# Performance work log

Hardware: AMD Instinct MI355X
Metric: run time of the kernel (lower is better)

The kernel has to match this reference:

```python
import jax, jax.numpy as jnp
import numpy as np

GENOMES, BATCH, SEQ, EMBED = 8, 2, 2048, 1024
HEADS, KV_HEADS = 16, 4
HEAD_DIM = EMBED // HEADS  # 64
RATIO = HEADS // KV_HEADS  # 4
CONSTANT = 10000.0


def _rope_tables(seq_len, head_dim, constant):
    theta = constant ** (-2.0 * jnp.arange(0, head_dim, 2, dtype=jnp.float32) / head_dim)
    angles = jnp.arange(seq_len, dtype=jnp.float32)[:, None] * theta[None, :]  # [S, hd/2]
    return jnp.cos(angles), jnp.sin(angles)


def _apply_rope(x, cos, sin):
    # x: [g,b,s,h,hd]; treat last dim as hd/2 complex pairs, rotate by angle per (s, pair)
    g, b, s, h, hd = x.shape
    xr = x.reshape(g, b, s, h, hd // 2, 2)
    x0, x1 = xr[..., 0], xr[..., 1]
    c = cos[None, None, :, None, :]
    sn = sin[None, None, :, None, :]
    o0 = x0 * c - x1 * sn
    o1 = x0 * sn + x1 * c
    return jnp.stack([o0, o1], axis=-1).reshape(g, b, s, h, hd)


def setup_inputs() -> dict:
    key = jax.random.key(0)
    ks = jax.random.split(key, 5)
    scale = 0.02
    return {
        "tensor": jax.random.normal(ks[0], (GENOMES, BATCH, SEQ, EMBED), dtype=jnp.float32),
        "Wq": jax.random.normal(ks[1], (GENOMES, EMBED, HEADS * HEAD_DIM), dtype=jnp.float32) * scale,
        "Wk": jax.random.normal(ks[2], (GENOMES, EMBED, KV_HEADS * HEAD_DIM), dtype=jnp.float32) * scale,
        "Wv": jax.random.normal(ks[3], (GENOMES, EMBED, KV_HEADS * HEAD_DIM), dtype=jnp.float32) * scale,
        "Wo": jax.random.normal(ks[4], (GENOMES, EMBED, EMBED), dtype=jnp.float32) * scale,
    }


def reference(tensor, Wq, Wk, Wv, Wo):
    g, b, s, _ = tensor.shape
    cos, sin = _rope_tables(SEQ, HEAD_DIM, CONSTANT)
    # per-genome linear projections
    q = jnp.einsum('gbsi,gio->gbso', tensor, Wq).reshape(g, b, s, HEADS, HEAD_DIM)
    k = jnp.einsum('gbsi,gio->gbso', tensor, Wk).reshape(g, b, s, KV_HEADS, HEAD_DIM)
    v = jnp.einsum('gbsi,gio->gbso', tensor, Wv).reshape(g, b, s, KV_HEADS, HEAD_DIM)
    q = _apply_rope(q, cos, sin)
    k = _apply_rope(k, cos, sin)
    # repeat_kv: [g,b,s,kvh,hd] -> [g,b,s,kvh*ratio,hd]
    k = jnp.broadcast_to(k[:, :, :, :, None, :], (g, b, s, KV_HEADS, RATIO, HEAD_DIM)).reshape(g, b, s, HEADS, HEAD_DIM)
    v = jnp.broadcast_to(v[:, :, :, :, None, :], (g, b, s, KV_HEADS, RATIO, HEAD_DIM)).reshape(g, b, s, HEADS, HEAD_DIM)
    # NOTE: faithful to the original (non-standard) einsums: contraction over seq in QK^T,
    # energy is [g,b,h,head_dim,head_dim]
    energy = jnp.einsum('gbshq,gbshk->gbhqk', q, k)
    scores = jax.nn.softmax(energy / jnp.sqrt(jnp.float32(HEAD_DIM)), axis=-1)
    # attention = value scaled by total score mass per (g,b,h)
    attention = jnp.einsum('gbhqk,gbshv->gbshv', scores, v)
    attention = attention.reshape(g, b, s, EMBED)
    return jnp.einsum('gbsi,gio->gbso', attention, Wo)
```

## Files before the change

### kernel.cpp

```cpp
#include <hip/hip_runtime.h>
#include <stdint.h>

#define GENOMES 8
#define BATCH 2
#define SEQ 2048
#define EMBED 1024
#define KVD 256
#define M_PER_G (BATCH*SEQ)

typedef float f32x4 __attribute__((ext_vector_type(4)));
typedef __bf16 bf16x8 __attribute__((ext_vector_type(8)));
typedef short s16x8 __attribute__((ext_vector_type(8)));
typedef short s16x4 __attribute__((ext_vector_type(4)));

static __device__ __forceinline__ unsigned short f2bf(float f) {
  unsigned int u = __builtin_bit_cast(unsigned int, f);
  u += 0x7FFFu + ((u >> 16) & 1u);
  return (unsigned short)(u >> 16);
}

__global__ __launch_bounds__(256) void wvt_kernel(const float* __restrict__ Wv,
                                                  unsigned short* __restrict__ WvT) {
  int g = blockIdx.y;
  int it = blockIdx.x >> 2;
  int ot = blockIdx.x & 3;
  int i0 = it * 64, o0 = ot * 64;
  const float* W = Wv + (size_t)g * EMBED * KVD;
  unsigned short* T = WvT + (size_t)g * KVD * EMBED;
  __shared__ unsigned short tl[64][65];
  int t = threadIdx.x;
  int rr = t >> 4;
  int cc = (t & 15) * 4;
#pragma unroll
  for (int p = 0; p < 4; ++p) {
    int r = rr + p * 16;
    float4 v = *(const float4*)(W + (size_t)(i0 + r) * KVD + o0 + cc);
    tl[r][cc + 0] = f2bf(v.x);
    tl[r][cc + 1] = f2bf(v.y);
    tl[r][cc + 2] = f2bf(v.z);
    tl[r][cc + 3] = f2bf(v.w);
  }
  __syncthreads();
#pragma unroll
  for (int p = 0; p < 4; ++p) {
    int o = rr + p * 16;
    s16x4 v;
    v[0] = (short)tl[cc + 0][o];
    v[1] = (short)tl[cc + 1][o];
    v[2] = (short)tl[cc + 2][o];
    v[3] = (short)tl[cc + 3][o];
    *(s16x4*)(T + (size_t)(o0 + o) * EMBED + i0 + cc) = v;
  }
}

__global__ __launch_bounds__(256) void rt_kernel(const float* __restrict__ Wo,
                                                 unsigned short* __restrict__ RT) {
  int g = blockIdx.y;
  int ot = blockIdx.x >> 2;
  int kh = blockIdx.x & 3;
  int o0 = ot * 64;
  const float* W = Wo + (size_t)g * EMBED * EMBED;
  unsigned short* T = RT + (size_t)g * EMBED * KVD;
  __shared__ float tl[64][65];
  int t = threadIdx.x;
  int rr = t >> 4;
  int cc = (t & 15) * 4;
#pragma unroll
  for (int p = 0; p < 4; ++p) {
    int d = rr + p * 16;
    float a0 = 0.f, a1 = 0.f, a2 = 0.f, a3 = 0.f;
#pragma unroll
    for (int r = 0; r < 4; ++r) {
      float4 v = *(const float4*)(W + (size_t)(kh * 256 + r * 64 + d) * EMBED + o0 + cc);
      a0 += v.x; a1 += v.y; a2 += v.z; a3 += v.w;
    }
    tl[d][cc + 0] = a0; tl[d][cc + 1] = a1; tl[d][cc + 2] = a2; tl[d][cc + 3] = a3;
  }
  __syncthreads();
#pragma unroll
  for (int p = 0; p < 4; ++p) {
    int o = rr + p * 16;
    s16x4 v;
    v[0] = (short)f2bf(64.f * tl[cc + 0][o]);
    v[1] = (short)f2bf(64.f * tl[cc + 1][o]);
    v[2] = (short)f2bf(64.f * tl[cc + 2][o]);
    v[3] = (short)f2bf(64.f * tl[cc + 3][o]);
    *(s16x4*)(T + (size_t)(o0 + o) * KVD + kh * 64 + cc) = v;
  }
}

template <bool A_F32, bool OUT_BF16, int M, int N, int K>
__global__ __launch_bounds__(256) void gemm_bt(const void* __restrict__ Aall,
                                               const unsigned short* __restrict__ Btall,
                                               void* __restrict__ Call) {
  constexpr int BK = 32;
  int g = blockIdx.y;
  constexpr int NTILES = N / 128;
  int bm = blockIdx.x / NTILES;
  int bn = blockIdx.x % NTILES;
  int m0 = bm * 128, n0 = bn * 128;
  const unsigned short* Bt = Btall + (size_t)g * N * K;
  const float* Af = (const float*)Aall + (size_t)g * M * K;
  const unsigned short* Ab = (const unsigned short*)Aall + (size_t)g * M * K;

  __shared__ unsigned short As[128][BK];
  __shared__ unsigned short Bs[128][BK];

  int t = threadIdx.x;
  int lane = t & 63, wave = t >> 6;
  int wm = (wave >> 1) * 64, wn = (wave & 1) * 64;
  int lm = lane & 15, quad = lane >> 4;
  int kq = quad * 8;

  f32x4 acc[4][4] = {};

  for (int k0 = 0; k0 < K; k0 += BK) {
    if constexpr (A_F32) {
      int row = t >> 3, col = (t & 7) * 4;
#pragma unroll
      for (int p = 0; p < 4; ++p) {
        int r = row + p * 32;
        float4 v = *(const float4*)(Af + (size_t)(m0 + r) * K + k0 + col);
        s16x4 b;
        b[0] = (short)f2bf(v.x); b[1] = (short)f2bf(v.y);
        b[2] = (short)f2bf(v.z); b[3] = (short)f2bf(v.w);
        *(s16x4*)&As[r][col] = b;
      }
    } else {
      int row = t >> 2, col = (t & 3) * 8;
#pragma unroll
      for (int p = 0; p < 2; ++p) {
        int r = row + p * 64;
        s16x8 v = *(const s16x8*)(Ab + (size_t)(m0 + r) * K + k0 + col);
        *(s16x8*)&As[r][col] = v;
      }
    }
    {
      int row = t >> 2, col = (t & 3) * 8;
#pragma unroll
      for (int p = 0; p < 2; ++p) {
        int r = row + p * 64;
        s16x8 v = *(const s16x8*)(Bt + (size_t)(n0 + r) * K + k0 + col);
        *(s16x8*)&Bs[r][col] = v;
      }
    }
    __syncthreads();

    bf16x8 af[4], bfr[4];
#pragma unroll
    for (int i = 0; i < 4; ++i) {
      af[i]  = __builtin_bit_cast(bf16x8, *(const s16x8*)&As[wm + i * 16 + lm][kq]);
      bfr[i] = __builtin_bit_cast(bf16x8, *(const s16x8*)&Bs[wn + i * 16 + lm][kq]);
    }
#pragma unroll
    for (int i = 0; i < 4; ++i)
#pragma unroll
      for (int j = 0; j < 4; ++j)
        acc[i][j] = __builtin_amdgcn_mfma_f32_16x16x32_bf16(af[i], bfr[j], acc[i][j], 0, 0, 0);
    __syncthreads();
  }

  if constexpr (OUT_BF16) {
    unsigned short* C = (unsigned short*)Call + (size_t)g * M * N;
#pragma unroll
    for (int i = 0; i < 4; ++i)
#pragma unroll
      for (int j = 0; j < 4; ++j)
#pragma unroll
        for (int r = 0; r < 4; ++r) {
          int mm = m0 + wm + i * 16 + quad * 4 + r;
          int nn = n0 + wn + j * 16 + lm;
          C[(size_t)mm * N + nn] = f2bf(acc[i][j][r]);
        }
  } else {
    float* C = (float*)Call + (size_t)g * M * N;
#pragma unroll
    for (int i = 0; i < 4; ++i)
#pragma unroll
      for (int j = 0; j < 4; ++j)
#pragma unroll
        for (int r = 0; r < 4; ++r) {
          int mm = m0 + wm + i * 16 + quad * 4 + r;
          int nn = n0 + wn + j * 16 + lm;
          C[(size_t)mm * N + nn] = acc[i][j][r];
        }
  }
}

extern "C" void kernel_launch(void* const* d_in, const int* in_sizes, int n_in,
                              void* d_out, int out_size, void* d_ws, size_t ws_size,
                              hipStream_t stream) {
  const float* tensor = (const float*)d_in[0];
  const float* Wv = (const float*)d_in[3];
  const float* Wo = (const float*)d_in[4];
  float* out = (float*)d_out;

  unsigned short* WvT = (unsigned short*)d_ws;
  unsigned short* RT  = WvT + (size_t)GENOMES * KVD * EMBED;
  unsigned short* V   = RT  + (size_t)GENOMES * EMBED * KVD;

  wvt_kernel<<<dim3(64, GENOMES), 256, 0, stream>>>(Wv, WvT);
  rt_kernel<<<dim3(64, GENOMES), 256, 0, stream>>>(Wo, RT);

  gemm_bt<true, true, M_PER_G, KVD, EMBED>
      <<<dim3((M_PER_G / 128) * (KVD / 128), GENOMES), 256, 0, stream>>>(tensor, WvT, V);

  gemm_bt<false, false, M_PER_G, EMBED, KVD>
      <<<dim3((M_PER_G / 128) * (EMBED / 128), GENOMES), 256, 0, stream>>>(V, RT, out);
}
```

Measured before the change: 331.0 us.

## Double-buffer GEMM tiles via direct global-to-LDS loads with XOR swizzle and XCD remap

Rewrites the batched GEMM mainloop to stage A and B tiles straight into LDS with global_load_lds into a double buffer, so the next tile's fetch overlaps the current MFMAs. The f32 activations are now stored raw in LDS and converted to bf16 at fragment-read time. LDS columns are XOR-swizzled to avoid bank conflicts, and block IDs are remapped across the 8 XCDs. The tile shrinks to 128x64 to raise the block count. The trade-off is double the LDS footprint and lower per-block reuse from the smaller N tile.

```diff
diff --git a/kernel.cpp b/kernel.cpp
--- a/kernel.cpp
+++ b/kernel.cpp
@@ -17,6 +17,12 @@
   unsigned int u = __builtin_bit_cast(unsigned int, f);
   u += 0x7FFFu + ((u >> 16) & 1u);
   return (unsigned short)(u >> 16);
+}
+
+static __device__ __forceinline__ void gll16(const void* g, void* l) {
+  __builtin_amdgcn_global_load_lds(
+      (const __attribute__((address_space(1))) unsigned int*)g,
+      (__attribute__((address_space(3))) unsigned int*)l, 16, 0, 0);
 }
 
 __global__ __launch_bounds__(256) void wvt_kernel(const float* __restrict__ Wv,
@@ -93,95 +99,139 @@
 __global__ __launch_bounds__(256) void gemm_bt(const void* __restrict__ Aall,
                                                const unsigned short* __restrict__ Btall,
                                                void* __restrict__ Call) {
-  constexpr int BK = 32;
+  constexpr int BM = 128, BN = 64, BK = 32;
+  constexpr int ABYTES = A_F32 ? BM * BK * 4 : BM * BK * 2;
+  constexpr int SB = ABYTES + BN * BK * 2;
+  constexpr int NTN = N / BN;
+  constexpr int NWG = (M / BM) * NTN;
+  constexpr int NT = K / BK;
+  static_assert(NWG % 8 == 0, "XCD swizzle needs nwg%8==0");
+
+  __shared__ __align__(16) unsigned char smem[2 * SB];
+
   int g = blockIdx.y;
-  constexpr int NTILES = N / 128;
-  int bm = blockIdx.x / NTILES;
-  int bn = blockIdx.x % NTILES;
-  int m0 = bm * 128, n0 = bn * 128;
+  int bid = blockIdx.x;
+  int lt = (bid & 7) * (NWG >> 3) + (bid >> 3);
+  int bm = lt / NTN, bn = lt % NTN;
+  int m0 = bm * BM, n0 = bn * BN;
+
   const unsigned short* Bt = Btall + (size_t)g * N * K;
   const float* Af = (const float*)Aall + (size_t)g * M * K;
   const unsigned short* Ab = (const unsigned short*)Aall + (size_t)g * M * K;
 
-  __shared__ unsigned short As[128][BK];
-  __shared__ unsigned short Bs[128][BK];
-
-  int t = threadIdx.x;
-  int lane = t & 63, wave = t >> 6;
-  int wm = (wave >> 1) * 64, wn = (wave & 1) * 64;
+  int tid = threadIdx.x;
+  int lane = tid & 63, wave = tid >> 6;
   int lm = lane & 15, quad = lane >> 4;
-  int kq = quad * 8;
-
-  f32x4 acc[4][4] = {};
-
-  for (int k0 = 0; k0 < K; k0 += BK) {
+  int wm = wave * 32;
+
+  const float* srcAf = nullptr;
+  const unsigned short* srcAb = nullptr;
+  if constexpr (A_F32) {
+    int rA = wave * 8 + (lane >> 3);
+    int cA = (lane & 7) ^ ((lane >> 3) & 7);
+    srcAf = Af + (size_t)(m0 + rA) * K + cA * 4;
+  } else {
+    int rA = wave * 16 + (lane >> 2);
+    int cA = (lane & 3) ^ ((lane >> 2) & 3);
+    srcAb = Ab + (size_t)(m0 + rA) * K + cA * 8;
+  }
+  int rB = wave * 16 + (lane >> 2);
+  int cB = (lane & 3) ^ ((lane >> 2) & 3);
+  const unsigned short* srcB = Bt + (size_t)(n0 + rB) * K + cB * 8;
+
+  int offA[2][2];
+  int offB[4];
+#pragma unroll
+  for (int i = 0; i < 2; ++i) {
     if constexpr (A_F32) {
-      int row = t >> 3, col = (t & 7) * 4;
-#pragma unroll
-      for (int p = 0; p < 4; ++p) {
-        int r = row + p * 32;
-        float4 v = *(const float4*)(Af + (size_t)(m0 + r) * K + k0 + col);
-        s16x4 b;
-        b[0] = (short)f2bf(v.x); b[1] = (short)f2bf(v.y);
-        b[2] = (short)f2bf(v.z); b[3] = (short)f2bf(v.w);
-        *(s16x4*)&As[r][col] = b;
+#pragma unroll
+      for (int u = 0; u < 2; ++u)
+        offA[i][u] = (wm + i * 16 + lm) * 128 + (((2 * quad + u) ^ (lm & 7)) * 16);
+    } else {
+      offA[i][0] = (wm + i * 16 + lm) * 64 + ((quad ^ (lm & 3)) * 16);
+    }
+  }
+#pragma unroll
+  for (int j = 0; j < 4; ++j)
+    offB[j] = ABYTES + (j * 16 + lm) * 64 + ((quad ^ (lm & 3)) * 16);
+
+  f32x4 acc[2][4] = {};
+
+  auto stage = [&](int buf, int t) {
+    unsigned char* db = smem + buf * SB;
+    if constexpr (A_F32) {
+      const float* s = srcAf + t * BK;
+#pragma unroll
+      for (int p = 0; p < 4; ++p)
+        gll16(s + (size_t)p * 32 * K, db + p * 4096 + wave * 1024);
+    } else {
+      const unsigned short* s = srcAb + t * BK;
+#pragma unroll
+      for (int p = 0; p < 2; ++p)
+        gll16(s + (size_t)p * 64 * K, db + p * 4096 + wave * 1024);
+    }
+    gll16(srcB + t * BK, db + ABYTES + wave * 1024);
+  };
+
+  stage(0, 0);
+  __syncthreads();
+
+  for (int t = 0; t < NT; ++t) {
+    if (t + 1 < NT) stage((t + 1) & 1, t + 1);
+
+    const unsigned char* db = smem + (t & 1) * SB;
+    bf16x8 a[2], b[4];
+    if constexpr (A_F32) {
+#pragma unroll
+      for (int i = 0; i < 2; ++i) {
+        f32x4 lo = *(const f32x4*)(db + offA[i][0]);
+        f32x4 hi = *(const f32x4*)(db + offA[i][1]);
+#pragma unroll
+        for (int u = 0; u < 4; ++u) {
+          a[i][u] = (__bf16)lo[u];
+          a[i][4 + u] = (__bf16)hi[u];
+        }
       }
     } else {
-      int row = t >> 2, col = (t & 3) * 8;
-#pragma unroll
-      for (int p = 0; p < 2; ++p) {
-        int r = row + p * 64;
-        s16x8 v = *(const s16x8*)(Ab + (size_t)(m0 + r) * K + k0 + col);
-        *(s16x8*)&As[r][col] = v;
-      }
-    }
-    {
-      int row = t >> 2, col = (t & 3) * 8;
-#pragma unroll
-      for (int p = 0; p < 2; ++p) {
-        int r = row + p * 64;
-        s16x8 v = *(const s16x8*)(Bt + (size_t)(n0 + r) * K + k0 + col);
-        *(s16x8*)&Bs[r][col] = v;
-      }
-    }
-    __syncthreads();
-
-    bf16x8 af[4], bfr[4];
-#pragma unroll
-    for (int i = 0; i < 4; ++i) {
-      af[i]  = __builtin_bit_cast(bf16x8, *(const s16x8*)&As[wm + i * 16 + lm][kq]);
-      bfr[i] = __builtin_bit_cast(bf16x8, *(const s16x8*)&Bs[wn + i * 16 + lm][kq]);
-    }
-#pragma unroll
-    for (int i = 0; i < 4; ++i)
+#pragma unroll
+      for (int i = 0; i < 2; ++i)
+        a[i] = __builtin_bit_cast(bf16x8, *(const s16x8*)(db + offA[i][0]));
+    }
+#pragma unroll
+    for (int j = 0; j < 4; ++j)
+      b[j] = __builtin_bit_cast(bf16x8, *(const s16x8*)(db + offB[j]));
+
+#pragma unroll
+    for (int i = 0; i < 2; ++i)
 #pragma unroll
       for (int j = 0; j < 4; ++j)
-        acc[i][j] = __builtin_amdgcn_mfma_f32_16x16x32_bf16(af[i], bfr[j], acc[i][j], 0, 0, 0);
+        acc[i][j] = __builtin_amdgcn_mfma_f32_16x16x32_bf16(a[i], b[j], acc[i][j], 0, 0, 0);
+
     __syncthreads();
   }
 
   if constexpr (OUT_BF16) {
     unsigned short* C = (unsigned short*)Call + (size_t)g * M * N;
 #pragma unroll
-    for (int i = 0; i < 4; ++i)
+    for (int i = 0; i < 2; ++i)
 #pragma unroll
       for (int j = 0; j < 4; ++j)
 #pragma unroll
         for (int r = 0; r < 4; ++r) {
           int mm = m0 + wm + i * 16 + quad * 4 + r;
-          int nn = n0 + wn + j * 16 + lm;
+          int nn = n0 + j * 16 + lm;
           C[(size_t)mm * N + nn] = f2bf(acc[i][j][r]);
         }
   } else {
     float* C = (float*)Call + (size_t)g * M * N;
 #pragma unroll
-    for (int i = 0; i < 4; ++i)
+    for (int i = 0; i < 2; ++i)
 #pragma unroll
       for (int j = 0; j < 4; ++j)
 #pragma unroll
         for (int r = 0; r < 4; ++r) {
           int mm = m0 + wm + i * 16 + quad * 4 + r;
-          int nn = n0 + wn + j * 16 + lm;
+          int nn = n0 + j * 16 + lm;
           C[(size_t)mm * N + nn] = acc[i][j][r];
         }
   }
@@ -203,8 +253,8 @@
   rt_kernel<<<dim3(64, GENOMES), 256, 0, stream>>>(Wo, RT);
 
   gemm_bt<true, true, M_PER_G, KVD, EMBED>
-      <<<dim3((M_PER_G / 128) * (KVD / 128), GENOMES), 256, 0, stream>>>(tensor, WvT, V);
+      <<<dim3((M_PER_G / 128) * (KVD / 64), GENOMES), 256, 0, stream>>>(tensor, WvT, V);
 
   gemm_bt<false, false, M_PER_G, EMBED, KVD>
-      <<<dim3((M_PER_G / 128) * (EMBED / 128), GENOMES), 256, 0, stream>>>(V, RT, out);
-}
+      <<<dim3((M_PER_G / 128) * (EMBED / 64), GENOMES), 256, 0, stream>>>(V, RT, out);
+}
```

After: 335.1 us. About the same (+1.2%).

## Restructure GEMM into 64x256 tiles with register-prefetched B and double-buffered A

Applied to the files above, without the earlier changes.

The GEMM kernel moves from 128x128 tiles with both operands staged in shared memory to 64x256 tiles. B fragments are now loaded straight from global memory into registers one step ahead, and A is double-buffered in shared memory with an XOR swizzle and prefetched two steps ahead. It also adds an XCD-aware block-index swizzle and a single lgkmcnt barrier per k-step. The aim is to overlap global loads with MFMA work and cut LDS traffic and sync count. The cost is higher register pressure and uncoalesced per-lane B loads, which may lower occupancy.

```diff
diff --git a/kernel.cpp b/kernel.cpp
--- a/kernel.cpp
+++ b/kernel.cpp
@@ -18,6 +18,12 @@
   u += 0x7FFFu + ((u >> 16) & 1u);
   return (unsigned short)(u >> 16);
 }
+
+#define LGKM_BARRIER() do { \
+  asm volatile("s_waitcnt lgkmcnt(0)" ::: "memory"); \
+  __builtin_amdgcn_s_barrier(); \
+  asm volatile("" ::: "memory"); \
+} while (0)
 
 __global__ __launch_bounds__(256) void wvt_kernel(const float* __restrict__ Wv,
                                                   unsigned short* __restrict__ WvT) {
@@ -93,71 +99,112 @@
 __global__ __launch_bounds__(256) void gemm_bt(const void* __restrict__ Aall,
                                                const unsigned short* __restrict__ Btall,
                                                void* __restrict__ Call) {
-  constexpr int BK = 32;
+  constexpr int BM = 64, BN = 256, BK = 32;
+  constexpr int NTN = N / BN;
+  constexpr int NWG = (M / BM) * NTN;
+  constexpr int NT = K / BK;
+  static_assert(NWG % 8 == 0, "XCD swizzle needs nwg%8==0");
+  static_assert(NT % 2 == 0 && NT >= 4, "manual 2-unroll + 2-ahead A prefetch");
+
+  __shared__ __align__(16) unsigned char As[2][BM * BK * 2];
+
   int g = blockIdx.y;
-  constexpr int NTILES = N / 128;
-  int bm = blockIdx.x / NTILES;
-  int bn = blockIdx.x % NTILES;
-  int m0 = bm * 128, n0 = bn * 128;
+  int bid = blockIdx.x;
+  int lt = (bid & 7) * (NWG >> 3) + (bid >> 3);
+  int bm = lt / NTN, bn = lt % NTN;
+  int m0 = bm * BM, n0 = bn * BN;
+
   const unsigned short* Bt = Btall + (size_t)g * N * K;
   const float* Af = (const float*)Aall + (size_t)g * M * K;
   const unsigned short* Ab = (const unsigned short*)Aall + (size_t)g * M * K;
 
-  __shared__ unsigned short As[128][BK];
-  __shared__ unsigned short Bs[128][BK];
-
-  int t = threadIdx.x;
-  int lane = t & 63, wave = t >> 6;
-  int wm = (wave >> 1) * 64, wn = (wave & 1) * 64;
+  int tid = threadIdx.x;
+  int lane = tid & 63, wave = tid >> 6;
   int lm = lane & 15, quad = lane >> 4;
-  int kq = quad * 8;
+  int wn = wave * 64;
+
+  int srow = tid >> 2, sc4 = tid & 3;
+  int sdst = srow * 64 + ((sc4 ^ (srow & 3)) * 16);
+  const float* gAf = Af + (size_t)(m0 + srow) * K + sc4 * 8;
+  const unsigned short* gAb = Ab + (size_t)(m0 + srow) * K + sc4 * 8;
+
+  int offA[4];
+#pragma unroll
+  for (int i = 0; i < 4; ++i) {
+    int row = i * 16 + lm;
+    offA[i] = row * 64 + ((quad ^ (row & 3)) * 16);
+  }
+
+  const unsigned short* gB[4];
+#pragma unroll
+  for (int j = 0; j < 4; ++j)
+    gB[j] = Bt + (size_t)(n0 + wn + j * 16 + lm) * K + quad * 8;
 
   f32x4 acc[4][4] = {};
 
-  for (int k0 = 0; k0 < K; k0 += BK) {
+  bf16x8 b0[4], b1[4];
+  f32x4 a0l, a0h, a1l, a1h;
+  s16x8 a0b, a1b;
+
+  auto loadA = [&](int h, f32x4& dl, f32x4& dh, s16x8& db) {
     if constexpr (A_F32) {
-      int row = t >> 3, col = (t & 7) * 4;
-#pragma unroll
-      for (int p = 0; p < 4; ++p) {
-        int r = row + p * 32;
-        float4 v = *(const float4*)(Af + (size_t)(m0 + r) * K + k0 + col);
-        s16x4 b;
-        b[0] = (short)f2bf(v.x); b[1] = (short)f2bf(v.y);
-        b[2] = (short)f2bf(v.z); b[3] = (short)f2bf(v.w);
-        *(s16x4*)&As[r][col] = b;
+      const float* s = gAf + (size_t)h * BK;
+      dl = *(const f32x4*)(s);
+      dh = *(const f32x4*)(s + 4);
+    } else {
+      db = *(const s16x8*)(gAb + (size_t)h * BK);
+    }
+  };
+  auto writeA = [&](int h, const f32x4& sl, const f32x4& sh, const s16x8& sb) {
+    s16x8 w;
+    if constexpr (A_F32) {
+#pragma unroll
+      for (int u = 0; u < 4; ++u) {
+        w[u] = (short)f2bf(sl[u]);
+        w[4 + u] = (short)f2bf(sh[u]);
       }
     } else {
-      int row = t >> 2, col = (t & 3) * 8;
-#pragma unroll
-      for (int p = 0; p < 2; ++p) {
-        int r = row + p * 64;
-        s16x8 v = *(const s16x8*)(Ab + (size_t)(m0 + r) * K + k0 + col);
-        *(s16x8*)&As[r][col] = v;
-      }
+      w = sb;
     }
-    {
-      int row = t >> 2, col = (t & 3) * 8;
-#pragma unroll
-      for (int p = 0; p < 2; ++p) {
-        int r = row + p * 64;
-        s16x8 v = *(const s16x8*)(Bt + (size_t)(n0 + r) * K + k0 + col);
-        *(s16x8*)&Bs[r][col] = v;
-      }
-    }
-    __syncthreads();
-
-    bf16x8 af[4], bfr[4];
-#pragma unroll
-    for (int i = 0; i < 4; ++i) {
-      af[i]  = __builtin_bit_cast(bf16x8, *(const s16x8*)&As[wm + i * 16 + lm][kq]);
-      bfr[i] = __builtin_bit_cast(bf16x8, *(const s16x8*)&Bs[wn + i * 16 + lm][kq]);
-    }
+    *(s16x8*)(&As[h & 1][sdst]) = w;
+  };
+  auto loadB = [&](int h, bf16x8 (&dst)[4]) {
+#pragma unroll
+    for (int j = 0; j < 4; ++j)
+      dst[j] = __builtin_bit_cast(bf16x8, *(const s16x8*)(gB[j] + (size_t)h * BK));
+  };
+
+  auto body = [&](int h, bf16x8 (&bcur)[4], bf16x8 (&bnxt)[4],
+                  f32x4& dl, f32x4& dh, s16x8& db,
+                  f32x4& sl, f32x4& sh, s16x8& sb) {
+    if (h + 1 < NT) loadB(h + 1, bnxt);
+    if (h + 2 < NT) loadA(h + 2, dl, dh, db);
+
+    const unsigned char* base = &As[h & 1][0];
+    bf16x8 a[4];
+#pragma unroll
+    for (int i = 0; i < 4; ++i)
+      a[i] = __builtin_bit_cast(bf16x8, *(const s16x8*)(base + offA[i]));
+
 #pragma unroll
     for (int i = 0; i < 4; ++i)
 #pragma unroll
       for (int j = 0; j < 4; ++j)
-        acc[i][j] = __builtin_amdgcn_mfma_f32_16x16x32_bf16(af[i], bfr[j], acc[i][j], 0, 0, 0);
-    __syncthreads();
+        acc[i][j] = __builtin_amdgcn_mfma_f32_16x16x32_bf16(a[i], bcur[j], acc[i][j], 0, 0, 0);
+
+    if (h + 1 < NT) writeA(h + 1, sl, sh, sb);
+    LGKM_BARRIER();
+  };
+
+  loadA(0, a0l, a0h, a0b);
+  loadA(1, a1l, a1h, a1b);
+  writeA(0, a0l, a0h, a0b);
+  loadB(0, b0);
+  LGKM_BARRIER();
+
+  for (int h = 0; h < NT; h += 2) {
+    body(h,     b0, b1, a0l, a0h, a0b, a1l, a1h, a1b);
+    body(h + 1, b1, b0, a1l, a1h, a1b, a0l, a0h, a0b);
   }
 
   if constexpr (OUT_BF16) {
@@ -168,7 +215,7 @@
       for (int j = 0; j < 4; ++j)
 #pragma unroll
         for (int r = 0; r < 4; ++r) {
-          int mm = m0 + wm + i * 16 + quad * 4 + r;
+          int mm = m0 + i * 16 + quad * 4 + r;
           int nn = n0 + wn + j * 16 + lm;
           C[(size_t)mm * N + nn] = f2bf(acc[i][j][r]);
         }
@@ -180,7 +227,7 @@
       for (int j = 0; j < 4; ++j)
 #pragma unroll
         for (int r = 0; r < 4; ++r) {
-          int mm = m0 + wm + i * 16 + quad * 4 + r;
+          int mm = m0 + i * 16 + quad * 4 + r;
           int nn = n0 + wn + j * 16 + lm;
           C[(size_t)mm * N + nn] = acc[i][j][r];
         }
@@ -203,8 +250,8 @@
   rt_kernel<<<dim3(64, GENOMES), 256, 0, stream>>>(Wo, RT);
 
   gemm_bt<true, true, M_PER_G, KVD, EMBED>
-      <<<dim3((M_PER_G / 128) * (KVD / 128), GENOMES), 256, 0, stream>>>(tensor, WvT, V);
+      <<<dim3((M_PER_G / 64) * (KVD / 256), GENOMES), 256, 0, stream>>>(tensor, WvT, V);
 
   gemm_bt<false, false, M_PER_G, EMBED, KVD>
-      <<<dim3((M_PER_G / 128) * (EMBED / 128), GENOMES), 256, 0, stream>>>(V, RT, out);
-}
+      <<<dim3((M_PER_G / 64) * (EMBED / 256), GENOMES), 256, 0, stream>>>(V, RT, out);
+}
```

After: 338.4 us. 2.2% more time.
